# Kernel optimization log

Measured on AMD Instinct MI355X. Metric: run time of the kernel, lower is better.

## Reference

```python
import jax, jax.numpy as jnp
import numpy as np

DIM = 4096
N_HEADS = 32
N_KV_HEADS = 8
HEAD_DIM = DIM // N_HEADS          # 128
N_REPS = N_HEADS // N_KV_HEADS    # 4
MAX_SEQ = 2048
SEQ = 2048
BSZ = 1
ROPE_THETA = 500000.0
NEG_INF = -1e9


def _make_freqs():
    inv = 1.0 / (ROPE_THETA ** (np.arange(0, HEAD_DIM, 2, dtype=np.float32) / HEAD_DIM))
    t = np.arange(MAX_SEQ, dtype=np.float32)
    f = np.outer(t, inv)  # [MAX_SEQ, HEAD_DIM//2]
    return jnp.asarray(np.cos(f)), jnp.asarray(np.sin(f))


def setup_inputs() -> dict:
    key = jax.random.key(0)
    ks = jax.random.split(key, 6)
    scale = 1.0 / np.sqrt(DIM)
    x = jax.random.normal(ks[0], (BSZ, SEQ, DIM), dtype=jnp.float32)
    wq = jax.random.normal(ks[1], (N_HEADS * HEAD_DIM, DIM), dtype=jnp.float32) * scale
    wk = jax.random.normal(ks[2], (N_KV_HEADS * HEAD_DIM, DIM), dtype=jnp.float32) * scale
    wv = jax.random.normal(ks[3], (N_KV_HEADS * HEAD_DIM, DIM), dtype=jnp.float32) * scale
    wo = jax.random.normal(ks[4], (DIM, N_HEADS * HEAD_DIM), dtype=jnp.float32) * scale
    freqs_cos, freqs_sin = _make_freqs()
    freqs_cos, freqs_sin = freqs_cos[:SEQ], freqs_sin[:SEQ]
    # causal additive mask [SEQ, SEQ]
    mask = jnp.where(jnp.tril(jnp.ones((SEQ, SEQ), dtype=bool)), 0.0, NEG_INF).astype(jnp.float32)
    return {"x": x, "wq": wq, "wk": wk, "wv": wv, "wo": wo,
            "freqs_cos": freqs_cos, "freqs_sin": freqs_sin,
            "mask": mask, "start_pos": 0}


def _apply_rope(t, cos, sin):
    # t: [b, s, h, d]; cos/sin: [s, d//2]
    b, s, h, d = t.shape
    tr = t.reshape(b, s, h, d // 2, 2)
    re, im = tr[..., 0], tr[..., 1]
    c = cos[None, :, None, :]
    sn = sin[None, :, None, :]
    out = jnp.stack([re * c - im * sn, re * sn + im * c], axis=-1)
    return out.reshape(b, s, h, d)


def reference(x, wq, wk, wv, wo, freqs_cos, freqs_sin, mask, start_pos):
    b, s, _ = x.shape
    xq = (x @ wq.T).reshape(b, s, N_HEADS, HEAD_DIM)
    xk = (x @ wk.T).reshape(b, s, N_KV_HEADS, HEAD_DIM)
    xv = (x @ wv.T).reshape(b, s, N_KV_HEADS, HEAD_DIM)
    xq = _apply_rope(xq, freqs_cos, freqs_sin)
    xk = _apply_rope(xk, freqs_cos, freqs_sin)
    # KV cache write + read (start_pos is a static Python int)
    kv_len = start_pos + s
    k_cache = jnp.zeros((b, MAX_SEQ, N_KV_HEADS, HEAD_DIM), dtype=x.dtype)
    v_cache = jnp.zeros((b, MAX_SEQ, N_KV_HEADS, HEAD_DIM), dtype=x.dtype)
    k_cache = jax.lax.dynamic_update_slice(k_cache, xk, (0, start_pos, 0, 0))
    v_cache = jax.lax.dynamic_update_slice(v_cache, xv, (0, start_pos, 0, 0))
    keys = k_cache[:, :kv_len]   # [b, kv, Hkv, d]
    vals = v_cache[:, :kv_len]
    # GQA expand (repeat_interleave over kv heads)
    keys = jnp.broadcast_to(keys[:, :, :, None, :], (b, kv_len, N_KV_HEADS, N_REPS, HEAD_DIM)).reshape(b, kv_len, N_HEADS, HEAD_DIM)
    vals = jnp.broadcast_to(vals[:, :, :, None, :], (b, kv_len, N_KV_HEADS, N_REPS, HEAD_DIM)).reshape(b, kv_len, N_HEADS, HEAD_DIM)
    scores = jnp.einsum('bqhd,bkhd->bhqk', xq, keys) / jnp.sqrt(jnp.float32(HEAD_DIM))
    scores = scores + mask[None, None, :, :]
    probs = jax.nn.softmax(scores.astype(jnp.float32), axis=-1).astype(xq.dtype)
    out = jnp.einsum('bhqk,bkhd->bqhd', probs, vals).reshape(b, s, N_HEADS * HEAD_DIM)
    return out @ wo.T
```

## Files before the change

### kernel.cpp

```cpp
#include <hip/hip_runtime.h>

#define SEQ   2048
#define DIM   4096
#define NH    32
#define NKV   8
#define HD    128
#define KVDIM 1024

typedef __attribute__((ext_vector_type(8))) short bf16x8;
typedef __attribute__((ext_vector_type(4))) float f32x4;

static __device__ __forceinline__ unsigned short f2bf(float x) {
    unsigned int u = __float_as_uint(x);
    unsigned int r = (u + 0x7fffu + ((u >> 16) & 1u)) >> 16;
    return (unsigned short)r;
}

#define N_X4   2097152
#define B0_4   2097152
#define B1_4   6291456
#define B2_4   7340032
#define B3_4   8388608
#define TOT4  12582912

__global__ __launch_bounds__(256) void cvt5_kernel(const float* __restrict__ x,
                                                   const float* __restrict__ wq,
                                                   const float* __restrict__ wk,
                                                   const float* __restrict__ wv,
                                                   const float* __restrict__ wo,
                                                   unsigned short* __restrict__ d)
{
    int i = blockIdx.x * 256 + threadIdx.x;
    const int stride = gridDim.x * 256;
    for (; i < TOT4; i += stride) {
        const float* s; int off;
        if      (i < B0_4) { s = x;  off = i;         }
        else if (i < B1_4) { s = wq; off = i - B0_4;  }
        else if (i < B2_4) { s = wk; off = i - B1_4;  }
        else if (i < B3_4) { s = wv; off = i - B2_4;  }
        else               { s = wo; off = i - B3_4;  }
        float4 v = reinterpret_cast<const float4*>(s)[off];
        ushort4 u;
        u.x = f2bf(v.x); u.y = f2bf(v.y); u.z = f2bf(v.z); u.w = f2bf(v.w);
        reinterpret_cast<ushort4*>(d)[i] = u;
    }
}

__global__ __launch_bounds__(256) void cvt_kernel(const float* __restrict__ s,
                                                  unsigned short* __restrict__ d, int n4)
{
    int i = blockIdx.x * 256 + threadIdx.x;
    int stride = gridDim.x * 256;
    for (; i < n4; i += stride) {
        float4 v = reinterpret_cast<const float4*>(s)[i];
        ushort4 u;
        u.x = f2bf(v.x); u.y = f2bf(v.y); u.z = f2bf(v.z); u.w = f2bf(v.w);
        reinterpret_cast<ushort4*>(d)[i] = u;
    }
}

template<bool ABF, bool WBF, int MODE>
__global__ __launch_bounds__(256) void gemm_bt(
    const void* __restrict__ Ap, const void* __restrict__ Wp,
    void* __restrict__ Cp, void* __restrict__ Cp2, void* __restrict__ Cp3, int ldC,
    const float* __restrict__ cosT, const float* __restrict__ sinT)
{
    constexpr bool DB = ABF && WBF;
    constexpr int AS = ABF ? 32 : 40;
    constexpr int BS = WBF ? 32 : 40;
    __shared__ unsigned short As[DB ? 2 : 1][128 * AS];
    __shared__ unsigned short Bs[DB ? 2 : 1][128 * BS];

    const int t  = threadIdx.x;
    const int w  = t >> 6, l = t & 63;
    const int lr = l & 15, lg = l >> 4;
    const int wm = (w >> 1) * 64, wn = (w & 1) * 64;

    const int gx  = gridDim.x;
    const int nwg = gx * gridDim.y;
    int flat = blockIdx.y * gx + blockIdx.x;
    if ((nwg & 7) == 0) flat = (flat & 7) * (nwg >> 3) + (flat >> 3);
    const int m0 = (flat / gx) * 128, n0 = (flat % gx) * 128;

    f32x4 acc[4][4] = {};

    if constexpr (DB) {
        const unsigned short* A = (const unsigned short*)Ap;
        const unsigned short* B = (const unsigned short*)Wp;

        auto STAGE = [&](int k0, int b) {
            #pragma unroll
            for (int i = 0; i < 2; ++i) {
                const unsigned short* src =
                    A + (size_t)(m0 + i * 64 + w * 16 + (l >> 2)) * 4096 + k0 + (l & 3) * 8;
                __builtin_amdgcn_global_load_lds(
                    (const __attribute__((address_space(1))) void*)src,
                    (__attribute__((address_space(3))) void*)&As[b][(i * 64 + w * 16) * 32],
                    16, 0, 0);
            }
            #pragma unroll
            for (int i = 0; i < 2; ++i) {
                const unsigned short* src =
                    B + (size_t)(n0 + i * 64 + w * 16 + (l >> 2)) * 4096 + k0 + (l & 3) * 8;
                __builtin_amdgcn_global_load_lds(
                    (const __attribute__((address_space(1))) void*)src,
                    (__attribute__((address_space(3))) void*)&Bs[b][(i * 64 + w * 16) * 32],
                    16, 0, 0);
            }
        };

        STAGE(0, 0);
        __syncthreads();
        int cur = 0;
        for (int k0 = 0; k0 < 4096; k0 += 32) {
            if (k0 + 32 < 4096) STAGE(k0 + 32, cur ^ 1);

            bf16x8 af[4], bfr[4];
            #pragma unroll
            for (int m = 0; m < 4; ++m)
                af[m] = *reinterpret_cast<const bf16x8*>(&As[cur][(wm + m * 16 + lr) * 32 + lg * 8]);
            #pragma unroll
            for (int n = 0; n < 4; ++n)
                bfr[n] = *reinterpret_cast<const bf16x8*>(&Bs[cur][(wn + n * 16 + lr) * 32 + lg * 8]);
            #pragma unroll
            for (int m = 0; m < 4; ++m)
                #pragma unroll
                for (int n = 0; n < 4; ++n)
                    acc[m][n] = __builtin_amdgcn_mfma_f32_16x16x32_bf16(af[m], bfr[n], acc[m][n], 0, 0, 0);
            __syncthreads();
            cur ^= 1;
        }
    } else {
        for (int k0 = 0; k0 < 4096; k0 += 32) {
            {
                const float* A = (const float*)Ap;
                #pragma unroll
                for (int i = 0; i < 4; ++i) {
                    int row = (t >> 3) + 32 * i, kc = (t & 7) * 4;
                    float4 v = *reinterpret_cast<const float4*>(A + (size_t)(m0 + row) * 4096 + k0 + kc);
                    ushort4 u;
                    u.x = f2bf(v.x); u.y = f2bf(v.y); u.z = f2bf(v.z); u.w = f2bf(v.w);
                    *reinterpret_cast<ushort4*>(&As[0][row * 40 + kc]) = u;
                }
            }
            {
                const float* B = (const float*)Wp;
                #pragma unroll
                for (int i = 0; i < 4; ++i) {
                    int row = (t >> 3) + 32 * i, kc = (t & 7) * 4;
                    float4 v = *reinterpret_cast<const float4*>(B + (size_t)(n0 + row) * 4096 + k0 + kc);
                    ushort4 u;
                    u.x = f2bf(v.x); u.y = f2bf(v.y); u.z = f2bf(v.z); u.w = f2bf(v.w);
                    *reinterpret_cast<ushort4*>(&Bs[0][row * 40 + kc]) = u;
                }
            }
            __syncthreads();

            bf16x8 af[4], bfr[4];
            #pragma unroll
            for (int m = 0; m < 4; ++m)
                af[m] = *reinterpret_cast<const bf16x8*>(&As[0][(wm + m * 16 + lr) * AS + lg * 8]);
            #pragma unroll
            for (int n = 0; n < 4; ++n)
                bfr[n] = *reinterpret_cast<const bf16x8*>(&Bs[0][(wn + n * 16 + lr) * BS + lg * 8]);
            #pragma unroll
            for (int m = 0; m < 4; ++m)
                #pragma unroll
                for (int n = 0; n < 4; ++n)
                    acc[m][n] = __builtin_amdgcn_mfma_f32_16x16x32_bf16(af[m], bfr[n], acc[m][n], 0, 0, 0);
            __syncthreads();
        }
    }

    if constexpr (MODE == 3) {
        float* C = (float*)Cp;
        #pragma unroll
        for (int m = 0; m < 4; ++m)
            #pragma unroll
            for (int n = 0; n < 4; ++n)
                #pragma unroll
                for (int j = 0; j < 4; ++j)
                    C[(size_t)(m0 + wm + m * 16 + lg * 4 + j) * ldC + n0 + wn + n * 16 + lr] =
                        acc[m][n][j];
    } else if constexpr (MODE == 2) {
        unsigned short* VT = (unsigned short*)Cp;
        #pragma unroll
        for (int m = 0; m < 4; ++m)
            #pragma unroll
            for (int n = 0; n < 4; ++n) {
                int col = n0 + wn + n * 16 + lr;
                int r0  = m0 + wm + m * 16 + lg * 4;
                ushort4 u;
                u.x = f2bf(acc[m][n][0]); u.y = f2bf(acc[m][n][1]);
                u.z = f2bf(acc[m][n][2]); u.w = f2bf(acc[m][n][3]);
                *reinterpret_cast<ushort4*>(&VT[(size_t)col * SEQ + r0]) = u;
            }
    } else if constexpr (MODE == 1) {
        unsigned short* C = (unsigned short*)Cp;
        #pragma unroll
        for (int m = 0; m < 4; ++m)
            #pragma unroll
            for (int n = 0; n < 4; ++n) {
                int col = n0 + wn + n * 16 + lr;
                int p   = (col & 127) >> 1;
                float sg = (col & 1) ? 1.f : -1.f;
                #pragma unroll
                for (int j = 0; j < 4; ++j) {
                    int row = m0 + wm + m * 16 + lg * 4 + j;
                    float v  = acc[m][n][j];
                    float pr = __shfl_xor(v, 1);
                    float o  = v * cosT[row * 64 + p] + sg * sinT[row * 64 + p] * pr;
                    C[(size_t)row * ldC + col] = f2bf(o);
                }
            }
    } else {
        if (n0 < 5120) {
            unsigned short* C;
            int ldc2, csub;
            if (n0 < 4096) { C = (unsigned short*)Cp;  ldc2 = DIM;   csub = 0;    }
            else           { C = (unsigned short*)Cp2; ldc2 = KVDIM; csub = 4096; }
            #pragma unroll
            for (int m = 0; m < 4; ++m)
                #pragma unroll
                for (int n = 0; n < 4; ++n) {
                    int col = n0 + wn + n * 16 + lr - csub;
                    int p   = (col & 127) >> 1;
                    float sg = (col & 1) ? 1.f : -1.f;
                    #pragma unroll
                    for (int j = 0; j < 4; ++j) {
                        int row = m0 + wm + m * 16 + lg * 4 + j;
                        float v  = acc[m][n][j];
                        float pr = __shfl_xor(v, 1);
                        float o  = v * cosT[row * 64 + p] + sg * sinT[row * 64 + p] * pr;
                        C[(size_t)row * ldc2 + col] = f2bf(o);
                    }
                }
        } else {
            unsigned short* VT = (unsigned short*)Cp3;
            #pragma unroll
            for (int m = 0; m < 4; ++m)
                #pragma unroll
                for (int n = 0; n < 4; ++n) {
                    int col = n0 + wn + n * 16 + lr - 5120;
                    int r0  = m0 + wm + m * 16 + lg * 4;
                    ushort4 u;
                    u.x = f2bf(acc[m][n][0]); u.y = f2bf(acc[m][n][1]);
                    u.z = f2bf(acc[m][n][2]); u.w = f2bf(acc[m][n][3]);
                    *reinterpret_cast<ushort4*>(&VT[(size_t)col * SEQ + r0]) = u;
                }
        }
    }
}

__global__ __launch_bounds__(512, 4) void attn_kernel(const unsigned short* __restrict__ Qb,
                                                      const unsigned short* __restrict__ Kb,
                                                      const unsigned short* __restrict__ Vt,
                                                      unsigned short* __restrict__ Ob)
{
    __shared__ unsigned short Kl[2][64 * 128];
    __shared__ unsigned short Vl[2][128 * 64];
    __shared__ unsigned short Pl[8][16 * 64];

    const int t  = threadIdx.x;
    const int w  = t >> 6, l = t & 63;
    const int lr = l & 15, lg = l >> 4;
    const int qb = (gridDim.x - 1) - blockIdx.x;
    const int h  = blockIdx.y;
    const int kvh = h >> 2;
    const int qw = qb * 128 + w * 16;

    bf16x8 qf[4];
    #pragma unroll
    for (int f = 0; f < 4; ++f)
        qf[f] = *reinterpret_cast<const bf16x8*>(Qb + (size_t)(qw + lr) * DIM + h * HD + f * 32 + lg * 8);

    f32x4 po[8] = {};
    float lsum[4] = {0.f, 0.f, 0.f, 0.f};
    const float scale = 0.08838834764831845f;
    const int nt = 2 * qb + 2;

    auto STAGE = [&](int kt, int b) {
        const int kbase = kt * 64;
        #pragma unroll
        for (int i = 0; i < 2; ++i) {
            int key = w * 8 + 4 * i + (l >> 4);
            const unsigned short* src = Kb + (size_t)(kbase + key) * KVDIM + kvh * HD
                                           + (((l & 15) ^ (key & 7)) << 3);
            __builtin_amdgcn_global_load_lds(
                (const __attribute__((address_space(1))) void*)src,
                (__attribute__((address_space(3))) void*)&Kl[b][(w * 8 + 4 * i) * 128],
                16, 0, 0);
        }
        #pragma unroll
        for (int i = 0; i < 2; ++i) {
            int d = w * 16 + 8 * i + (l >> 3);
            const unsigned short* src = Vt + (size_t)(kvh * HD + d) * SEQ + kbase
                                           + (((l & 7) ^ (d & 7)) << 3);
            __builtin_amdgcn_global_load_lds(
                (const __attribute__((address_space(1))) void*)src,
                (__attribute__((address_space(3))) void*)&Vl[b][(w * 16 + 8 * i) * 64],
                16, 0, 0);
        }
    };

    STAGE(0, 0);
    __syncthreads();
    int cur = 0;

    for (int kt = 0; kt < nt; ++kt) {
        const int kbase = kt * 64;
        if (kt + 1 < nt) STAGE(kt + 1, cur ^ 1);

        if (kbase <= qw + 15) {
            f32x4 sc[4] = {};
            #pragma unroll
            for (int c = 0; c < 4; ++c) {
                int key = c * 16 + lr;
                #pragma unroll
                for (int f = 0; f < 4; ++f) {
                    bf16x8 kb = *reinterpret_cast<const bf16x8*>(
                        &Kl[cur][(key * 128 + f * 32 + lg * 8) ^ ((key & 7) << 3)]);
                    sc[c] = __builtin_amdgcn_mfma_f32_16x16x32_bf16(qf[f], kb, sc[c], 0, 0, 0);
                }
            }

            const bool diag = (kbase + 63 > qw);
            #pragma unroll
            for (int j = 0; j < 4; ++j) {
                int q = qw + lg * 4 + j;
                int prow = lg * 4 + j;
                float ps = 0.f;
                #pragma unroll
                for (int c = 0; c < 4; ++c) {
                    float p = __expf(sc[c][j] * scale - 8.0f);
                    if (diag && (kbase + c * 16 + lr > q)) p = 0.f;
                    ps += p;
                    Pl[w][(prow * 64 + c * 16 + lr) ^ ((prow & 7) << 3)] = f2bf(p);
                }
                lsum[j] += ps;
            }

            bf16x8 pa0 = *reinterpret_cast<const bf16x8*>(
                &Pl[w][(lr * 64 + lg * 8) ^ ((lr & 7) << 3)]);
            bf16x8 pa1 = *reinterpret_cast<const bf16x8*>(
                &Pl[w][(lr * 64 + 32 + lg * 8) ^ ((lr & 7) << 3)]);
            #pragma unroll
            for (int o = 0; o < 8; ++o) {
                int d = o * 16 + lr;
                bf16x8 bv0 = *reinterpret_cast<const bf16x8*>(
                    &Vl[cur][(d * 64 + lg * 8) ^ ((d & 7) << 3)]);
                bf16x8 bv1 = *reinterpret_cast<const bf16x8*>(
                    &Vl[cur][(d * 64 + 32 + lg * 8) ^ ((d & 7) << 3)]);
                po[o] = __builtin_amdgcn_mfma_f32_16x16x32_bf16(pa0, bv0, po[o], 0, 0, 0);
                po[o] = __builtin_amdgcn_mfma_f32_16x16x32_bf16(pa1, bv1, po[o], 0, 0, 0);
            }
        }
        __syncthreads();
        cur ^= 1;
    }

    #pragma unroll
    for (int j = 0; j < 4; ++j) {
        float s = lsum[j];
        s += __shfl_xor(s, 1);
        s += __shfl_xor(s, 2);
        s += __shfl_xor(s, 4);
        s += __shfl_xor(s, 8);
        float inv = 1.f / s;
        int q = qw + lg * 4 + j;
        #pragma unroll
        for (int o = 0; o < 8; ++o)
            Ob[(size_t)q * DIM + h * HD + o * 16 + lr] = f2bf(po[o][j] * inv);
    }
}

extern "C" void kernel_launch(void* const* d_in, const int* in_sizes, int n_in,
                              void* d_out, int out_size, void* d_ws, size_t ws_size,
                              hipStream_t stream) {
    const float* x    = (const float*)d_in[0];
    const float* wq   = (const float*)d_in[1];
    const float* wk   = (const float*)d_in[2];
    const float* wv   = (const float*)d_in[3];
    const float* wo   = (const float*)d_in[4];
    const float* cosT = (const float*)d_in[5];
    const float* sinT = (const float*)d_in[6];
    float* out = (float*)d_out;

    unsigned short* ws = (unsigned short*)d_ws;
    const bool big = ws_size >= (size_t)136 * 1024 * 1024;

    if (big) {
        unsigned short* xb   = ws;
        unsigned short* wqkv = xb   + (size_t)SEQ * DIM;
        unsigned short* wob  = wqkv + (size_t)(DIM + 2 * KVDIM) * DIM;
        unsigned short* Qb   = wob  + (size_t)DIM * DIM;
        unsigned short* Kb   = Qb   + (size_t)SEQ * DIM;
        unsigned short* Vtb  = Kb   + (size_t)SEQ * KVDIM;
        unsigned short* Ob   = Vtb  + (size_t)KVDIM * SEQ;

        cvt5_kernel<<<2048, 256, 0, stream>>>(x, wq, wk, wv, wo, ws);

        gemm_bt<true, true, 5><<<dim3(48, 16), 256, 0, stream>>>(
            xb, wqkv, Qb, Kb, Vtb, 0, cosT, sinT);
        attn_kernel<<<dim3(16, 32), 512, 0, stream>>>(Qb, Kb, Vtb, Ob);
        gemm_bt<true, true, 3><<<dim3(32, 16), 256, 0, stream>>>(
            Ob, wob, out, nullptr, nullptr, DIM, nullptr, nullptr);
    } else {
        unsigned short* Qb  = ws;
        unsigned short* Kb  = Qb  + (size_t)SEQ * DIM;
        unsigned short* Vtb = Kb  + (size_t)SEQ * KVDIM;
        unsigned short* Ob  = Vtb + (size_t)KVDIM * SEQ;

        gemm_bt<false, false, 1><<<dim3(32, 16), 256, 0, stream>>>(
            x, wq, Qb, nullptr, nullptr, DIM, cosT, sinT);
        gemm_bt<false, false, 1><<<dim3(8, 16),  256, 0, stream>>>(
            x, wk, Kb, nullptr, nullptr, KVDIM, cosT, sinT);
        gemm_bt<false, false, 2><<<dim3(8, 16),  256, 0, stream>>>(
            x, wv, Vtb, nullptr, nullptr, 0, nullptr, nullptr);
        attn_kernel<<<dim3(16, 32), 512, 0, stream>>>(Qb, Kb, Vtb, Ob);
        gemm_bt<true, false, 3><<<dim3(32, 16), 256, 0, stream>>>(
            Ob, wo, out, nullptr, nullptr, DIM, nullptr, nullptr);
    }
}
```

Baseline: 638.4 us.

## Unroll bf16 GEMM k-loop by two, drop block swizzle, stage fp32 output via LDS

The double-buffered bf16 GEMM main loop now handles two k-steps per iteration with fixed buffer indices instead of a runtime toggle. The XCD-aware block-index swizzle is replaced by plain blockIdx mapping. For fp32 output (MODE 3), accumulators are first written to LDS in 32-row chunks and then stored to global memory as coalesced float4 rows instead of scattered scalar stores. Dropping the swizzle may hurt L2 locality across chiplets, and the staged epilogue adds extra barriers.

```diff
diff --git a/kernel.cpp b/kernel.cpp
--- a/kernel.cpp
+++ b/kernel.cpp
@@ -16,7 +16,6 @@
     return (unsigned short)r;
 }
 
-#define N_X4   2097152
 #define B0_4   2097152
 #define B1_4   6291456
 #define B2_4   7340032
@@ -75,12 +74,7 @@
     const int w  = t >> 6, l = t & 63;
     const int lr = l & 15, lg = l >> 4;
     const int wm = (w >> 1) * 64, wn = (w & 1) * 64;
-
-    const int gx  = gridDim.x;
-    const int nwg = gx * gridDim.y;
-    int flat = blockIdx.y * gx + blockIdx.x;
-    if ((nwg & 7) == 0) flat = (flat & 7) * (nwg >> 3) + (flat >> 3);
-    const int m0 = (flat / gx) * 128, n0 = (flat % gx) * 128;
+    const int m0 = blockIdx.y * 128, n0 = blockIdx.x * 128;
 
     f32x4 acc[4][4] = {};
 
@@ -108,27 +102,30 @@
                     16, 0, 0);
             }
         };
+        auto COMPUTE = [&](int b) {
+            bf16x8 af[4], bfr[4];
+            #pragma unroll
+            for (int m = 0; m < 4; ++m)
+                af[m] = *reinterpret_cast<const bf16x8*>(&As[b][(wm + m * 16 + lr) * 32 + lg * 8]);
+            #pragma unroll
+            for (int n = 0; n < 4; ++n)
+                bfr[n] = *reinterpret_cast<const bf16x8*>(&Bs[b][(wn + n * 16 + lr) * 32 + lg * 8]);
+            #pragma unroll
+            for (int m = 0; m < 4; ++m)
+                #pragma unroll
+                for (int n = 0; n < 4; ++n)
+                    acc[m][n] = __builtin_amdgcn_mfma_f32_16x16x32_bf16(af[m], bfr[n], acc[m][n], 0, 0, 0);
+        };
 
         STAGE(0, 0);
         __syncthreads();
-        int cur = 0;
-        for (int k0 = 0; k0 < 4096; k0 += 32) {
-            if (k0 + 32 < 4096) STAGE(k0 + 32, cur ^ 1);
-
-            bf16x8 af[4], bfr[4];
-            #pragma unroll
-            for (int m = 0; m < 4; ++m)
-                af[m] = *reinterpret_cast<const bf16x8*>(&As[cur][(wm + m * 16 + lr) * 32 + lg * 8]);
-            #pragma unroll
-            for (int n = 0; n < 4; ++n)
-                bfr[n] = *reinterpret_cast<const bf16x8*>(&Bs[cur][(wn + n * 16 + lr) * 32 + lg * 8]);
-            #pragma unroll
-            for (int m = 0; m < 4; ++m)
-                #pragma unroll
-                for (int n = 0; n < 4; ++n)
-                    acc[m][n] = __builtin_amdgcn_mfma_f32_16x16x32_bf16(af[m], bfr[n], acc[m][n], 0, 0, 0);
+        for (int k0 = 0; k0 < 4096; k0 += 64) {
+            STAGE(k0 + 32, 1);
+            COMPUTE(0);
             __syncthreads();
-            cur ^= 1;
+            if (k0 + 64 < 4096) STAGE(k0 + 64, 0);
+            COMPUTE(1);
+            __syncthreads();
         }
     } else {
         for (int k0 = 0; k0 < 4096; k0 += 32) {
@@ -174,14 +171,45 @@
 
     if constexpr (MODE == 3) {
         float* C = (float*)Cp;
-        #pragma unroll
-        for (int m = 0; m < 4; ++m)
-            #pragma unroll
-            for (int n = 0; n < 4; ++n)
-                #pragma unroll
-                for (int j = 0; j < 4; ++j)
-                    C[(size_t)(m0 + wm + m * 16 + lg * 4 + j) * ldC + n0 + wn + n * 16 + lr] =
-                        acc[m][n][j];
+        if constexpr (DB) {
+            float* Cl = reinterpret_cast<float*>(&As[0][0]);
+            #pragma unroll
+            for (int chunk = 0; chunk < 4; ++chunk) {
+                __syncthreads();
+                int mb = chunk * 32 - wm;
+                if (mb == 0 || mb == 32) {
+                    #pragma unroll
+                    for (int mm = 0; mm < 2; ++mm) {
+                        int m = (mb >> 4) + mm;
+                        #pragma unroll
+                        for (int n = 0; n < 4; ++n) {
+                            int col = wn + n * 16 + lr;
+                            #pragma unroll
+                            for (int j = 0; j < 4; ++j)
+                                Cl[(mm * 16 + lg * 4 + j) * 128 + col] = acc[m][n][j];
+                        }
+                    }
+                }
+                __syncthreads();
+                #pragma unroll
+                for (int p = 0; p < 4; ++p) {
+                    int r  = (t >> 5) + p * 8;
+                    int cc = (t & 31) * 4;
+                    float4 v = *reinterpret_cast<const float4*>(&Cl[r * 128 + cc]);
+                    *reinterpret_cast<float4*>(
+                        &C[(size_t)(m0 + chunk * 32 + r) * ldC + n0 + cc]) = v;
+                }
+            }
+        } else {
+            #pragma unroll
+            for (int m = 0; m < 4; ++m)
+                #pragma unroll
+                for (int n = 0; n < 4; ++n)
+                    #pragma unroll
+                    for (int j = 0; j < 4; ++j)
+                        C[(size_t)(m0 + wm + m * 16 + lg * 4 + j) * ldC + n0 + wn + n * 16 + lr] =
+                            acc[m][n][j];
+        }
     } else if constexpr (MODE == 2) {
         unsigned short* VT = (unsigned short*)Cp;
         #pragma unroll
```

Result: faster. 613.9 us (-3.8%).
